# Kernel tuning notes

Hardware: AMD Instinct MI355X
Metric: run time of the kernel (lower is better)

Reference implementation:

```python
import jax, jax.numpy as jnp
import numpy as np
from jax import lax

NEG = -1e9
B, H, C, TX, TY = 4, 256, 80, 256, 1024  # batch, hidden, mel bins, text len, mel len


def setup_inputs() -> dict:
    key = jax.random.key(0)
    k = jax.random.split(key, 6)
    en = jax.random.normal(k[0], (B, H, TX), jnp.float32)
    mu = jax.random.normal(k[1], (B, C, TX), jnp.float32)
    log_sigma = 0.1 * jax.random.normal(k[2], (B, C, TX), jnp.float32)
    y = jax.random.normal(k[3], (B, C, TY), jnp.float32)
    x_lengths = jax.random.randint(k[4], (B,), TX // 2, TX + 1, jnp.int32)
    y_lengths = jax.random.randint(k[5], (B,), TY // 2, TY + 1, jnp.int32)
    return {"en": en, "mu": mu, "log_sigma": log_sigma, "y": y,
            "x_lengths": x_lengths, "y_lengths": y_lengths}


def sequence_mask(lengths, max_len):
    return jnp.arange(max_len)[None, :] < lengths[:, None]


def compute_log_probs(mu, log_sigma, y):
    # y: [B,C,Ty] -> [B,1,Ty,C]; mu/log_sigma: [B,C,Tx] -> [B,Tx,1,C]
    yb = jnp.transpose(y, (0, 2, 1))[:, None]
    mub = jnp.transpose(mu, (0, 2, 1))[:, :, None]
    lsb = jnp.transpose(log_sigma, (0, 2, 1))[:, :, None]
    # mse / sigma^2 = (y-mu)^2 * exp(-2*log_sigma); mean over channel dim
    expo = -0.5 * jnp.mean((yb - mub) ** 2 * jnp.exp(-2.0 * lsb), axis=-1)  # [B,Tx,Ty]
    return expo - 0.5 * jnp.mean(lsb, axis=-1)  # broadcast [B,Tx,1] -> [B,Tx,Ty]


def maximum_path(logp, mask, x_lengths, y_lengths):
    """Monotonic alignment search (Glow-TTS Viterbi DP), vectorized over batch."""
    b, tx, ty = logp.shape
    lp = jnp.where(mask > 0, logp, NEG)
    cols = jnp.moveaxis(lp, 2, 0)  # [Ty, B, Tx]
    v0 = jnp.broadcast_to(jnp.where(jnp.arange(tx) == 0, 0.0, NEG), (b, tx)).astype(logp.dtype)

    def fwd(v, col):
        v_shift = jnp.concatenate([jnp.full((b, 1), NEG, v.dtype), v[:, :-1]], axis=1)
        diag = v_shift > v  # come from (x-1, y-1) rather than (x, y-1)
        return col + jnp.maximum(v, v_shift), diag

    _, diags = lax.scan(fwd, v0, cols)  # diags: [Ty, B, Tx] bool

    xs_idx = jnp.arange(tx)

    def bwd(idx, inp):
        yv, dcol = inp
        active = yv < y_lengths  # [B]
        row = (xs_idx[None, :] == idx[:, None]) & active[:, None]
        d = jnp.take_along_axis(dcol, idx[:, None], axis=1)[:, 0]
        idx = jnp.where(active & (idx > 0) & d, idx - 1, idx)
        return idx, row

    _, rows = lax.scan(bwd, x_lengths - 1, (jnp.arange(ty), diags), reverse=True)
    return lax.stop_gradient(jnp.moveaxis(rows, 0, 2).astype(logp.dtype))  # [B,Tx,Ty]


def generate_path(dr, mask):
    # dr: [B,Tx] durations; mask: [B,Tx,Ty]
    ty = mask.shape[-1]
    cum = jnp.cumsum(dr, axis=1)
    pm = (jnp.arange(ty)[None, None, :] < cum[:, :, None]).astype(dr.dtype)
    path = pm - jnp.pad(pm, ((0, 0), (1, 0), (0, 0)))[:, :-1]
    return path * mask


def reference(en, mu, log_sigma, y, x_lengths, y_lengths):
    tx, ty = mu.shape[-1], y.shape[-1]
    x_mask = sequence_mask(x_lengths, tx).astype(jnp.float32)  # [B,Tx]
    y_mask = sequence_mask(y_lengths, ty).astype(jnp.float32)  # [B,Ty]
    attn_mask = x_mask[:, :, None] * y_mask[:, None, :]        # [B,Tx,Ty]
    logp = compute_log_probs(mu, log_sigma, y)
    attn = maximum_path(logp, attn_mask, x_lengths, y_lengths)
    dr_mas = jnp.sum(attn, axis=-1)                            # durations [B,Tx]
    path = generate_path(dr_mas, attn_mask)                    # convert_dr_to_align
    # expand_encoder_outputs: attn^T @ en^T -> [B,H,Ty]
    o_en_ex = jnp.einsum('bxy,bhx->bhy', path, en)
    return o_en_ex, logp, attn, dr_mas
```

## Files before the change

kernel.cpp:

```cpp
#include <hip/hip_runtime.h>
#include <cstdint>
#include <cmath>

#define B_ 4
#define H_ 256
#define C_ 80
#define TX_ 256
#define TY_ 1024
#define NC_ 64
#define NEGF (-1e9f)

#define OFF_LOGP (B_*H_*TY_)
#define OFF_ATTN (OFF_LOGP + B_*TX_*TY_)
#define OFF_DR   (OFF_ATTN + B_*TX_*TY_)

__device__ __forceinline__ float dpp_shr1_negfill_f32(float x) {
  union { float f; int i; } u, o, r;
  u.f = x; o.f = NEGF;
  r.i = __builtin_amdgcn_update_dpp(o.i, u.i, 0x138, 0xf, 0xf, false);
  return r.f;
}

__global__ __launch_bounds__(256) void k_logp(
    const float* __restrict__ mu, const float* __restrict__ ls,
    const float* __restrict__ y, const int* __restrict__ xlp,
    const int* __restrict__ ylp, float* __restrict__ logp_out,
    float* __restrict__ lpT)
{
  const int b  = blockIdx.y;
  const int x0 = blockIdx.x * 4;
  const int tid = threadIdx.x;
  __shared__ double s_w[4][C_];
  __shared__ double s_m1[4][C_];
  __shared__ double s_wm2[4][C_];
  __shared__ double s_lsv[4][C_];
  __shared__ double s_K[4];
  __shared__ double s_t0[4];
  __shared__ float tile[TY_][4];
  for (int i = tid; i < 4 * C_; i += 256) {
    int xi = i / C_, c = i - xi * C_;
    double m = (double)mu[(b * C_ + c) * TX_ + x0 + xi];
    double l = (double)ls[(b * C_ + c) * TX_ + x0 + xi];
    double w = exp(-2.0 * l);
    s_w[xi][c]   = w;
    s_m1[xi][c]  = -2.0 * w * m;
    s_wm2[xi][c] = w * m * m;
    s_lsv[xi][c] = l;
  }
  __syncthreads();
  {
    int xi = tid >> 6, cc = tid & 63;
    double kp = (cc < C_) ? s_wm2[xi][cc] : 0.0;
    double tp = (cc < C_) ? s_lsv[xi][cc] : 0.0;
    if (cc + 64 < C_) { kp += s_wm2[xi][cc + 64]; tp += s_lsv[xi][cc + 64]; }
#pragma unroll
    for (int off = 32; off; off >>= 1) {
      kp += __shfl_down(kp, off);
      tp += __shfl_down(tp, off);
    }
    if (cc == 0) { s_K[xi] = kp; s_t0[xi] = -0.5 * (tp * (1.0 / C_)); }
  }
  __syncthreads();

  const int t0 = tid * 4;
  double acc[4][4];
#pragma unroll
  for (int xi = 0; xi < 4; ++xi)
#pragma unroll
    for (int k = 0; k < 4; ++k) acc[xi][k] = 0.0;

  const float4* yp = (const float4*)(y + (size_t)b * C_ * TY_) + tid;
#pragma unroll 4
  for (int c = 0; c < C_; ++c) {
    float4 yv = yp[c * (TY_ / 4)];
    double y0 = yv.x, y1 = yv.y, y2 = yv.z, y3 = yv.w;
#pragma unroll
    for (int xi = 0; xi < 4; ++xi) {
      double w = s_w[xi][c], m1 = s_m1[xi][c];
      double u0 = fma(w, y0, m1), u1 = fma(w, y1, m1);
      double u2 = fma(w, y2, m1), u3 = fma(w, y3, m1);
      acc[xi][0] = fma(u0, y0, acc[xi][0]);
      acc[xi][1] = fma(u1, y1, acc[xi][1]);
      acc[xi][2] = fma(u2, y2, acc[xi][2]);
      acc[xi][3] = fma(u3, y3, acc[xi][3]);
    }
  }

  const int xlen = xlp[b], ylen = ylp[b];
#pragma unroll
  for (int xi = 0; xi < 4; ++xi) {
    int x = x0 + xi;
    double c0 = s_t0[xi], K = s_K[xi];
    float r[4];
#pragma unroll
    for (int k = 0; k < 4; ++k)
      r[k] = (float)((acc[xi][k] + K) * (-0.5 / C_) + c0);
    *(float4*)&logp_out[((size_t)(b * TX_ + x)) * TY_ + t0] =
        make_float4(r[0], r[1], r[2], r[3]);
    bool xm = x < xlen;
#pragma unroll
    for (int k = 0; k < 4; ++k)
      tile[t0 + k][xi] = (xm && (t0 + k) < ylen) ? r[k] : NEGF;
  }
  __syncthreads();

  float* dst = lpT + (size_t)b * TY_ * TX_ + x0;
  const float4* tp = (const float4*)tile;
#pragma unroll
  for (int k = 0; k < 4; ++k) {
    int t = tid + 256 * k;
    *(float4*)&dst[(size_t)t * TX_] = tp[t];
  }
}

__global__ __launch_bounds__(64, 1) void k_dp(
    const float* __restrict__ lpT, const int* __restrict__ xlp,
    const int* __restrict__ ylp, float* __restrict__ dr_out,
    int* __restrict__ cum_ws, int* __restrict__ xt_ws)
{
  const int b = blockIdx.x;
  const int lane = threadIdx.x;
  __shared__ uint32_t bits[8192];
  __shared__ uint32_t dur[TX_];

  const float4* src = (const float4*)(lpT + (size_t)b * TY_ * TX_) + lane;

  float v0 = (lane == 0) ? 0.0f : NEGF, v1 = NEGF, v2 = NEGF, v3 = NEGF;
  float sh = NEGF;
  uint32_t b0 = 0, b1 = 0, b2 = 0, b3 = 0;

  float4 BA[16], BB[16], BC[16];
#pragma unroll
  for (int i = 0; i < 16; ++i) BA[i] = src[i * 64];
#pragma unroll
  for (int i = 0; i < 16; ++i) BB[i] = src[(16 + i) * 64];

#define DP_BODY(CUR, LD, c)                                                  \
  {                                                                          \
    const int tl = ((c) + 2 < NC_ ? (c) + 2 : NC_ - 1) * 16;                 \
    _Pragma("unroll")                                                        \
    for (int i = 0; i < 16; ++i) LD[i] = src[(tl + i) * 64];                 \
    _Pragma("unroll")                                                        \
    for (int i = 0; i < 16; ++i) {                                           \
      const int t = (c) * 16 + i;                                            \
      const float vs0 = sh;                                                  \
      uint32_t bit = 1u << (t & 31);                                         \
      if (vs0 > v0) b0 |= bit;                                               \
      if (v0 > v1)  b1 |= bit;                                               \
      if (v1 > v2)  b2 |= bit;                                               \
      if (v2 > v3)  b3 |= bit;                                               \
      float nv3 = CUR[i].w + fmaxf(v3, v2);                                  \
      sh = dpp_shr1_negfill_f32(nv3);                                        \
      float nv2 = CUR[i].z + fmaxf(v2, v1);                                  \
      float nv1 = CUR[i].y + fmaxf(v1, v0);                                  \
      float nv0 = CUR[i].x + fmaxf(v0, vs0);                                 \
      v0 = nv0; v1 = nv1; v2 = nv2; v3 = nv3;                                \
      if ((t & 31) == 31) {                                                  \
        int w = t >> 5;                                                      \
        uint4 pk; pk.x = b0; pk.y = b1; pk.z = b2; pk.w = b3;                \
        *(uint4*)&bits[w * 256 + 4 * lane] = pk;                             \
        b0 = b1 = b2 = b3 = 0;                                               \
      }                                                                      \
    }                                                                        \
  }

  for (int c = 0; c < NC_; c += 3) {
    DP_BODY(BA, BC, c);
    if (c + 1 < NC_) DP_BODY(BB, BA, c + 1);
    if (c + 2 < NC_) DP_BODY(BC, BB, c + 2);
  }
#undef DP_BODY

#pragma unroll
  for (int j = 0; j < 4; ++j) dur[4 * lane + j] = 0;
  __syncthreads();

  const int xlen = xlp[b], ylen = ylp[b];
  if (lane == 0) {
    int idx = xlen - 1;
    int t = ylen - 1;
    while (t >= 0) {
      if (idx == 0) { dur[0] += (uint32_t)(t + 1); break; }
      int w = t >> 5, rr = t & 31;
      uint32_t word = bits[w * 256 + idx];
      word &= (rr == 31) ? 0xffffffffu : ((1u << (rr + 1)) - 1u);
      while (word == 0 && w > 0) { --w; word = bits[w * 256 + idx]; }
      if (word == 0) { dur[idx] += (uint32_t)(t + 1); break; }
      int bitpos = 31 - __builtin_clz(word);
      int tp = (w << 5) | bitpos;
      dur[idx] += (uint32_t)(t - tp + 1);
      --idx;
      t = tp - 1;
    }
  }
  __syncthreads();

  uint32_t d0 = dur[4 * lane], d1 = dur[4 * lane + 1];
  uint32_t d2 = dur[4 * lane + 2], d3 = dur[4 * lane + 3];
  uint32_t own = d0 + d1 + d2 + d3;
  uint32_t s = own;
#pragma unroll
  for (int off = 1; off < 64; off <<= 1) {
    uint32_t n = __shfl_up(s, off);
    if (lane >= off) s += n;
  }
  uint32_t base = s - own;
  uint32_t c0 = base + d0, c1 = c0 + d1, c2 = c1 + d2, c3 = c2 + d3;
  int x = 4 * lane;
  cum_ws[b * TX_ + x]     = (int)c0;
  cum_ws[b * TX_ + x + 1] = (int)c1;
  cum_ws[b * TX_ + x + 2] = (int)c2;
  cum_ws[b * TX_ + x + 3] = (int)c3;
  dr_out[b * TX_ + x]     = (float)d0;
  dr_out[b * TX_ + x + 1] = (float)d1;
  dr_out[b * TX_ + x + 2] = (float)d2;
  dr_out[b * TX_ + x + 3] = (float)d3;
  int* xt = xt_ws + b * TY_;
  for (uint32_t t = c0 - d0; t < c0; ++t) xt[t] = x;
  for (uint32_t t = c1 - d1; t < c1; ++t) xt[t] = x + 1;
  for (uint32_t t = c2 - d2; t < c2; ++t) xt[t] = x + 2;
  for (uint32_t t = c3 - d3; t < c3; ++t) xt[t] = x + 3;
}

__global__ __launch_bounds__(256) void k_epi(
    const int* __restrict__ cum_ws, const int* __restrict__ xt_ws,
    const float* __restrict__ en, const int* __restrict__ ylp,
    float* __restrict__ attn, float* __restrict__ oen)
{
  const int b = blockIdx.y, bx = blockIdx.x, tid = threadIdx.x;
  __shared__ float row[TX_];
  if (bx < TX_) {
    const int x = bx;
    int hi = cum_ws[b * TX_ + x];
    int lo = (x > 0) ? cum_ws[b * TX_ + x - 1] : 0;
    int t0 = tid * 4;
    float4 v;
    v.x = (t0     >= lo && t0     < hi) ? 1.f : 0.f;
    v.y = (t0 + 1 >= lo && t0 + 1 < hi) ? 1.f : 0.f;
    v.z = (t0 + 2 >= lo && t0 + 2 < hi) ? 1.f : 0.f;
    v.w = (t0 + 3 >= lo && t0 + 3 < hi) ? 1.f : 0.f;
    *(float4*)&attn[((size_t)(b * TX_ + x)) * TY_ + t0] = v;
  } else {
    const int h = bx - TX_;
    row[tid] = en[((size_t)(b * H_ + h)) * TX_ + tid];
    __syncthreads();
    const int ylen = ylp[b];
    int t0 = tid * 4;
    int4 xi = *(const int4*)&xt_ws[b * TY_ + t0];
    float4 v;
    v.x = (t0     < ylen) ? row[xi.x & (TX_ - 1)] : 0.f;
    v.y = (t0 + 1 < ylen) ? row[xi.y & (TX_ - 1)] : 0.f;
    v.z = (t0 + 2 < ylen) ? row[xi.z & (TX_ - 1)] : 0.f;
    v.w = (t0 + 3 < ylen) ? row[xi.w & (TX_ - 1)] : 0.f;
    *(float4*)&oen[((size_t)(b * H_ + h)) * TY_ + t0] = v;
  }
}

extern "C" void kernel_launch(void* const* d_in, const int* in_sizes, int n_in,
                              void* d_out, int out_size, void* d_ws, size_t ws_size,
                              hipStream_t stream)
{
  const float* en = (const float*)d_in[0];
  const float* mu = (const float*)d_in[1];
  const float* ls = (const float*)d_in[2];
  const float* y  = (const float*)d_in[3];
  const int*   xl = (const int*)d_in[4];
  const int*   yl = (const int*)d_in[5];

  float* out  = (float*)d_out;
  float* oen  = out;
  float* logp = out + OFF_LOGP;
  float* attn = out + OFF_ATTN;
  float* dr   = out + OFF_DR;

  int* cum = (int*)d_ws;
  int* xt  = cum + B_ * TX_;

  k_logp<<<dim3(TX_ / 4, B_),   256, 0, stream>>>(mu, ls, y, xl, yl, logp, attn);
  k_dp  <<<B_,                   64, 0, stream>>>(attn, xl, yl, dr, cum, xt);
  k_epi <<<dim3(TX_ + H_, B_),  256, 0, stream>>>(cum, xt, en, yl, attn, oen);
}
```

Before: 203.9 us.

## Hand-schedule DP prefetch with inline-asm loads into reserved VGPR banks

Replaces the compiler-scheduled triple-buffered float4 prefetch in the Viterbi DP kernel with inline-asm global_load_dwordx4 into two fixed banks of 64 VGPRs each (v128-v255), gated by explicit s_waitcnt vmcnt counts. Each 16-step chunk is copied out of its bank into a register array before the bank is refilled, so one chunk stays in flight while the current one is consumed. The goal is to keep memory latency off the serial DP recurrence without the compiler inserting conservative waits. In exchange it adds v_mov copy overhead, relies on hardcoded register clobbers and wait counts, and is fragile if the compiler's own loads change vmcnt accounting.

```diff
diff --git a/kernel.cpp b/kernel.cpp
--- a/kernel.cpp
+++ b/kernel.cpp
@@ -113,6 +113,98 @@
   }
 }
 
+#define ALLBANKS \
+  "v128","v129","v130","v131","v132","v133","v134","v135", \
+  "v136","v137","v138","v139","v140","v141","v142","v143", \
+  "v144","v145","v146","v147","v148","v149","v150","v151", \
+  "v152","v153","v154","v155","v156","v157","v158","v159", \
+  "v160","v161","v162","v163","v164","v165","v166","v167", \
+  "v168","v169","v170","v171","v172","v173","v174","v175", \
+  "v176","v177","v178","v179","v180","v181","v182","v183", \
+  "v184","v185","v186","v187","v188","v189","v190","v191", \
+  "v192","v193","v194","v195","v196","v197","v198","v199", \
+  "v200","v201","v202","v203","v204","v205","v206","v207", \
+  "v208","v209","v210","v211","v212","v213","v214","v215", \
+  "v216","v217","v218","v219","v220","v221","v222","v223", \
+  "v224","v225","v226","v227","v228","v229","v230","v231", \
+  "v232","v233","v234","v235","v236","v237","v238","v239", \
+  "v240","v241","v242","v243","v244","v245","v246","v247", \
+  "v248","v249","v250","v251","v252","v253","v254","v255"
+
+#define ISSUE_BANK(R0,R1,R2,R3)                                             \
+  asm volatile(                                                             \
+    "global_load_dwordx4 v[" #R0 ":" #R0 "+3], %0, off\n\t"                 \
+    "global_load_dwordx4 v[" #R0 "+4:" #R0 "+7], %0, off offset:1024\n\t"   \
+    "global_load_dwordx4 v[" #R0 "+8:" #R0 "+11], %0, off offset:2048\n\t"  \
+    "global_load_dwordx4 v[" #R0 "+12:" #R0 "+15], %0, off offset:3072\n\t" \
+    "global_load_dwordx4 v[" #R1 ":" #R1 "+3], %1, off\n\t"                 \
+    "global_load_dwordx4 v[" #R1 "+4:" #R1 "+7], %1, off offset:1024\n\t"   \
+    "global_load_dwordx4 v[" #R1 "+8:" #R1 "+11], %1, off offset:2048\n\t"  \
+    "global_load_dwordx4 v[" #R1 "+12:" #R1 "+15], %1, off offset:3072\n\t" \
+    "global_load_dwordx4 v[" #R2 ":" #R2 "+3], %2, off\n\t"                 \
+    "global_load_dwordx4 v[" #R2 "+4:" #R2 "+7], %2, off offset:1024\n\t"   \
+    "global_load_dwordx4 v[" #R2 "+8:" #R2 "+11], %2, off offset:2048\n\t"  \
+    "global_load_dwordx4 v[" #R2 "+12:" #R2 "+15], %2, off offset:3072\n\t" \
+    "global_load_dwordx4 v[" #R3 ":" #R3 "+3], %3, off\n\t"                 \
+    "global_load_dwordx4 v[" #R3 "+4:" #R3 "+7], %3, off offset:1024\n\t"   \
+    "global_load_dwordx4 v[" #R3 "+8:" #R3 "+11], %3, off offset:2048\n\t"  \
+    "global_load_dwordx4 v[" #R3 "+12:" #R3 "+15], %3, off offset:3072\n\t" \
+    :: "v"(q0), "v"(q1), "v"(q2), "v"(q3) : ALLBANKS)
+
+#define ISSUE_B0() ISSUE_BANK(128, 144, 160, 176)
+#define ISSUE_B1() ISSUE_BANK(192, 208, 224, 240)
+
+#define CP16(WAITSTR, R, c, o)                                              \
+  asm volatile(WAITSTR                                                      \
+    "v_mov_b32 %0, v[" #R "]\n\t"   "v_mov_b32 %1, v[" #R "+1]\n\t"         \
+    "v_mov_b32 %2, v[" #R "+2]\n\t" "v_mov_b32 %3, v[" #R "+3]\n\t"         \
+    "v_mov_b32 %4, v[" #R "+4]\n\t" "v_mov_b32 %5, v[" #R "+5]\n\t"         \
+    "v_mov_b32 %6, v[" #R "+6]\n\t" "v_mov_b32 %7, v[" #R "+7]\n\t"         \
+    "v_mov_b32 %8, v[" #R "+8]\n\t" "v_mov_b32 %9, v[" #R "+9]\n\t"         \
+    "v_mov_b32 %10, v[" #R "+10]\n\t" "v_mov_b32 %11, v[" #R "+11]\n\t"     \
+    "v_mov_b32 %12, v[" #R "+12]\n\t" "v_mov_b32 %13, v[" #R "+13]\n\t"     \
+    "v_mov_b32 %14, v[" #R "+14]\n\t" "v_mov_b32 %15, v[" #R "+15]"         \
+    : "=v"((c)[(o)+0]), "=v"((c)[(o)+1]), "=v"((c)[(o)+2]), "=v"((c)[(o)+3]),\
+      "=v"((c)[(o)+4]), "=v"((c)[(o)+5]), "=v"((c)[(o)+6]), "=v"((c)[(o)+7]),\
+      "=v"((c)[(o)+8]), "=v"((c)[(o)+9]), "=v"((c)[(o)+10]),"=v"((c)[(o)+11]),\
+      "=v"((c)[(o)+12]),"=v"((c)[(o)+13]),"=v"((c)[(o)+14]),"=v"((c)[(o)+15])\
+    :: ALLBANKS)
+
+#define COPYOUT_B0(WAITSTR, c)                                              \
+  CP16(WAITSTR, 128, c, 0);  CP16("", 144, c, 16);                          \
+  CP16("", 160, c, 32);      CP16("", 176, c, 48)
+#define COPYOUT_B1(WAITSTR, c)                                              \
+  CP16(WAITSTR, 192, c, 0);  CP16("", 208, c, 16);                          \
+  CP16("", 224, c, 32);      CP16("", 240, c, 48)
+
+#define ADV() { q0 += 4096; q1 += 4096; q2 += 4096; q3 += 4096; }
+
+#define CONSUME16C(c, k)                                                    \
+  {                                                                         \
+    const int sb = ((k) & 1) << 4;                                          \
+    _Pragma("unroll")                                                       \
+    for (int i = 0; i < 16; ++i) {                                          \
+      const float vs0 = sh;                                                 \
+      const uint32_t bit = 1u << (sb + i);                                  \
+      if (vs0 > v0) b0 |= bit;                                              \
+      if (v0 > v1)  b1 |= bit;                                              \
+      if (v1 > v2)  b2 |= bit;                                              \
+      if (v2 > v3)  b3 |= bit;                                              \
+      float nv3 = (c)[4*i+3] + fmaxf(v3, v2);                               \
+      sh = dpp_shr1_negfill_f32(nv3);                                       \
+      float nv2 = (c)[4*i+2] + fmaxf(v2, v1);                               \
+      float nv1 = (c)[4*i+1] + fmaxf(v1, v0);                               \
+      float nv0 = (c)[4*i+0] + fmaxf(v0, vs0);                              \
+      v0 = nv0; v1 = nv1; v2 = nv2; v3 = nv3;                               \
+    }                                                                       \
+    if ((k) & 1) {                                                          \
+      const int w = (k) >> 1;                                               \
+      uint4 pk; pk.x = b0; pk.y = b1; pk.z = b2; pk.w = b3;                 \
+      *(uint4*)&bits[w * 256 + 4 * lane] = pk;                              \
+      b0 = b1 = b2 = b3 = 0;                                                \
+    }                                                                       \
+  }
+
 __global__ __launch_bounds__(64, 1) void k_dp(
     const float* __restrict__ lpT, const int* __restrict__ xlp,
     const int* __restrict__ ylp, float* __restrict__ dr_out,
@@ -123,53 +215,32 @@
   __shared__ uint32_t bits[8192];
   __shared__ uint32_t dur[TX_];
 
-  const float4* src = (const float4*)(lpT + (size_t)b * TY_ * TX_) + lane;
+  const float* q0 = lpT + (size_t)b * TY_ * TX_ + 4 * lane;
+  const float* q1 = q0 + 1024;
+  const float* q2 = q0 + 2048;
+  const float* q3 = q0 + 3072;
 
   float v0 = (lane == 0) ? 0.0f : NEGF, v1 = NEGF, v2 = NEGF, v3 = NEGF;
   float sh = NEGF;
   uint32_t b0 = 0, b1 = 0, b2 = 0, b3 = 0;
-
-  float4 BA[16], BB[16], BC[16];
-#pragma unroll
-  for (int i = 0; i < 16; ++i) BA[i] = src[i * 64];
-#pragma unroll
-  for (int i = 0; i < 16; ++i) BB[i] = src[(16 + i) * 64];
-
-#define DP_BODY(CUR, LD, c)                                                  \
-  {                                                                          \
-    const int tl = ((c) + 2 < NC_ ? (c) + 2 : NC_ - 1) * 16;                 \
-    _Pragma("unroll")                                                        \
-    for (int i = 0; i < 16; ++i) LD[i] = src[(tl + i) * 64];                 \
-    _Pragma("unroll")                                                        \
-    for (int i = 0; i < 16; ++i) {                                           \
-      const int t = (c) * 16 + i;                                            \
-      const float vs0 = sh;                                                  \
-      uint32_t bit = 1u << (t & 31);                                         \
-      if (vs0 > v0) b0 |= bit;                                               \
-      if (v0 > v1)  b1 |= bit;                                               \
-      if (v1 > v2)  b2 |= bit;                                               \
-      if (v2 > v3)  b3 |= bit;                                               \
-      float nv3 = CUR[i].w + fmaxf(v3, v2);                                  \
-      sh = dpp_shr1_negfill_f32(nv3);                                        \
-      float nv2 = CUR[i].z + fmaxf(v2, v1);                                  \
-      float nv1 = CUR[i].y + fmaxf(v1, v0);                                  \
-      float nv0 = CUR[i].x + fmaxf(v0, vs0);                                 \
-      v0 = nv0; v1 = nv1; v2 = nv2; v3 = nv3;                                \
-      if ((t & 31) == 31) {                                                  \
-        int w = t >> 5;                                                      \
-        uint4 pk; pk.x = b0; pk.y = b1; pk.z = b2; pk.w = b3;                \
-        *(uint4*)&bits[w * 256 + 4 * lane] = pk;                             \
-        b0 = b1 = b2 = b3 = 0;                                               \
-      }                                                                      \
-    }                                                                        \
-  }
-
-  for (int c = 0; c < NC_; c += 3) {
-    DP_BODY(BA, BC, c);
-    if (c + 1 < NC_) DP_BODY(BB, BA, c + 1);
-    if (c + 2 < NC_) DP_BODY(BC, BB, c + 2);
-  }
-#undef DP_BODY
+  float c[64];
+
+  ISSUE_B0(); ADV();
+  ISSUE_B1(); ADV();
+
+  for (int p = 0; p < 62; p += 2) {
+    COPYOUT_B0("s_waitcnt vmcnt(16)\n\t", c);
+    ISSUE_B0(); ADV();
+    CONSUME16C(c, p);
+    COPYOUT_B1("s_waitcnt vmcnt(16)\n\t", c);
+    ISSUE_B1(); ADV();
+    CONSUME16C(c, p + 1);
+  }
+  COPYOUT_B0("s_waitcnt vmcnt(16)\n\t", c);
+  CONSUME16C(c, 62);
+  COPYOUT_B1("s_waitcnt vmcnt(0)\n\t", c);
+  CONSUME16C(c, 63);
+  asm volatile("s_waitcnt vmcnt(0)" ::: "memory");
 
 #pragma unroll
   for (int j = 0; j < 4; ++j) dur[4 * lane + j] = 0;
```

New measurement: 198.2 us. 2.8% less time.

## Wavefront-pipeline Viterbi DP across four waves with LDS boundary exchange

Applied to the files above, without the earlier changes.

The DP kernel goes from one 64-lane wave handling 4 text positions per lane to 256 threads with one text position each. The four waves work as a skewed pipeline over 16-step time chunks: each wave hands the values at its last lane to the next wave through a double-buffered LDS array and a barrier every phase. The aim is to shorten the serial per-step dependency chain and spread the global loads over more waves. In exchange it pays 69 workgroup barriers plus LDS traffic and a short pipeline fill and drain.

```diff
diff --git a/kernel.cpp b/kernel.cpp
--- a/kernel.cpp
+++ b/kernel.cpp
@@ -113,113 +113,121 @@
   }
 }
 
-__global__ __launch_bounds__(64, 1) void k_dp(
+#define PHASE_BAR() \
+  asm volatile("s_waitcnt lgkmcnt(0)\n\ts_barrier" ::: "memory")
+
+#define PHASEQ(FL, FC, q)                                                   \
+  {                                                                         \
+    const int cl = (q) - w;                                                 \
+    if (cl >= 0 && cl < NC_) {                                              \
+      const float* cb = gb + (size_t)cl * 16 * TX_ + tid;                   \
+      _Pragma("unroll")                                                     \
+      for (int i = 0; i < 16; ++i) FL[i] = cb[i * TX_];                     \
+    }                                                                       \
+    const int cc = (q) - 2 - w;                                             \
+    if (cc >= 0 && cc < NC_) {                                              \
+      if (cc == 0) { v = (tid == 0) ? 0.0f : NEGF; word = 0u; }             \
+      const uint32_t bitbase = 1u << ((cc & 1) << 4);                       \
+      float* wr = (lane == 63) ? &bdry[cc & 1][w + 1][0] : &dummy[lane];    \
+      const float* bp = &bdry[cc & 1][w][0];                                \
+      float bv[16];                                                         \
+      *(float4*)&bv[0]  = *(const float4*)(bp);                             \
+      *(float4*)&bv[4]  = *(const float4*)(bp + 4);                         \
+      *(float4*)&bv[8]  = *(const float4*)(bp + 8);                         \
+      *(float4*)&bv[12] = *(const float4*)(bp + 12);                        \
+      wr[0] = v;                                                            \
+      _Pragma("unroll")                                                     \
+      for (int i = 0; i < 16; ++i) {                                        \
+        float vl = dpp_shr1_negfill_f32(v);                                 \
+        if (amlane0) vl = bv[i];                                            \
+        if (vl > v) word |= (bitbase << i);                                 \
+        float nv = FC[i] + fmaxf(v, vl);                                    \
+        if (i < 15) wr[i + 1] = nv;                                         \
+        v = nv;                                                             \
+      }                                                                     \
+      if (cc & 1) { bits[(cc >> 1) * 256 + tid] = word; word = 0u; }        \
+    }                                                                       \
+    PHASE_BAR();                                                            \
+  }
+
+__global__ __launch_bounds__(256, 1) void k_dp(
     const float* __restrict__ lpT, const int* __restrict__ xlp,
     const int* __restrict__ ylp, float* __restrict__ dr_out,
     int* __restrict__ cum_ws, int* __restrict__ xt_ws)
 {
   const int b = blockIdx.x;
-  const int lane = threadIdx.x;
+  const int tid = threadIdx.x;
+  const int lane = tid & 63;
+  const int w = tid >> 6;
   __shared__ uint32_t bits[8192];
   __shared__ uint32_t dur[TX_];
-
-  const float4* src = (const float4*)(lpT + (size_t)b * TY_ * TX_) + lane;
-
-  float v0 = (lane == 0) ? 0.0f : NEGF, v1 = NEGF, v2 = NEGF, v3 = NEGF;
-  float sh = NEGF;
-  uint32_t b0 = 0, b1 = 0, b2 = 0, b3 = 0;
-
-  float4 BA[16], BB[16], BC[16];
-#pragma unroll
-  for (int i = 0; i < 16; ++i) BA[i] = src[i * 64];
-#pragma unroll
-  for (int i = 0; i < 16; ++i) BB[i] = src[(16 + i) * 64];
-
-#define DP_BODY(CUR, LD, c)                                                  \
-  {                                                                          \
-    const int tl = ((c) + 2 < NC_ ? (c) + 2 : NC_ - 1) * 16;                 \
-    _Pragma("unroll")                                                        \
-    for (int i = 0; i < 16; ++i) LD[i] = src[(tl + i) * 64];                 \
-    _Pragma("unroll")                                                        \
-    for (int i = 0; i < 16; ++i) {                                           \
-      const int t = (c) * 16 + i;                                            \
-      const float vs0 = sh;                                                  \
-      uint32_t bit = 1u << (t & 31);                                         \
-      if (vs0 > v0) b0 |= bit;                                               \
-      if (v0 > v1)  b1 |= bit;                                               \
-      if (v1 > v2)  b2 |= bit;                                               \
-      if (v2 > v3)  b3 |= bit;                                               \
-      float nv3 = CUR[i].w + fmaxf(v3, v2);                                  \
-      sh = dpp_shr1_negfill_f32(nv3);                                        \
-      float nv2 = CUR[i].z + fmaxf(v2, v1);                                  \
-      float nv1 = CUR[i].y + fmaxf(v1, v0);                                  \
-      float nv0 = CUR[i].x + fmaxf(v0, vs0);                                 \
-      v0 = nv0; v1 = nv1; v2 = nv2; v3 = nv3;                                \
-      if ((t & 31) == 31) {                                                  \
-        int w = t >> 5;                                                      \
-        uint4 pk; pk.x = b0; pk.y = b1; pk.z = b2; pk.w = b3;                \
-        *(uint4*)&bits[w * 256 + 4 * lane] = pk;                             \
-        b0 = b1 = b2 = b3 = 0;                                               \
-      }                                                                      \
-    }                                                                        \
-  }
-
-  for (int c = 0; c < NC_; c += 3) {
-    DP_BODY(BA, BC, c);
-    if (c + 1 < NC_) DP_BODY(BB, BA, c + 1);
-    if (c + 2 < NC_) DP_BODY(BC, BB, c + 2);
-  }
-#undef DP_BODY
-
-#pragma unroll
-  for (int j = 0; j < 4; ++j) dur[4 * lane + j] = 0;
+  __shared__ float bdry[2][5][16];
+  __shared__ float dummy[80];
+
+  const float* gb = lpT + (size_t)b * TY_ * TX_;
+  const bool amlane0 = (w > 0) && (lane == 0);
+
+  float v = NEGF;
+  uint32_t word = 0;
+  float f0[16], f1[16], f2[16];
+
+  for (int q = 0; q < 69; q += 3) {
+    PHASEQ(f0, f1, q);
+    PHASEQ(f1, f2, q + 1);
+    PHASEQ(f2, f0, q + 2);
+  }
+  __syncthreads();
+
+  dur[tid] = 0;
   __syncthreads();
 
   const int xlen = xlp[b], ylen = ylp[b];
-  if (lane == 0) {
+  if (tid == 0) {
     int idx = xlen - 1;
     int t = ylen - 1;
     while (t >= 0) {
-      if (idx == 0) { dur[0] += (uint32_t)(t + 1); break; }
-      int w = t >> 5, rr = t & 31;
-      uint32_t word = bits[w * 256 + idx];
-      word &= (rr == 31) ? 0xffffffffu : ((1u << (rr + 1)) - 1u);
-      while (word == 0 && w > 0) { --w; word = bits[w * 256 + idx]; }
-      if (word == 0) { dur[idx] += (uint32_t)(t + 1); break; }
-      int bitpos = 31 - __builtin_clz(word);
-      int tp = (w << 5) | bitpos;
-      dur[idx] += (uint32_t)(t - tp + 1);
+      if (idx == 0) { dur[0] = (uint32_t)(t + 1); break; }
+      int ww = t >> 5, rr = t & 31;
+      uint32_t wd = bits[ww * 256 + idx];
+      wd &= (rr == 31) ? 0xffffffffu : ((1u << (rr + 1)) - 1u);
+      while (wd == 0 && ww > 0) { --ww; wd = bits[ww * 256 + idx]; }
+      if (wd == 0) { dur[idx] = (uint32_t)(t + 1); break; }
+      int bitpos = 31 - __builtin_clz(wd);
+      int tp = (ww << 5) | bitpos;
+      dur[idx] = (uint32_t)(t - tp + 1);
       --idx;
       t = tp - 1;
     }
   }
   __syncthreads();
 
-  uint32_t d0 = dur[4 * lane], d1 = dur[4 * lane + 1];
-  uint32_t d2 = dur[4 * lane + 2], d3 = dur[4 * lane + 3];
-  uint32_t own = d0 + d1 + d2 + d3;
-  uint32_t s = own;
-#pragma unroll
-  for (int off = 1; off < 64; off <<= 1) {
-    uint32_t n = __shfl_up(s, off);
-    if (lane >= off) s += n;
-  }
-  uint32_t base = s - own;
-  uint32_t c0 = base + d0, c1 = c0 + d1, c2 = c1 + d2, c3 = c2 + d3;
-  int x = 4 * lane;
-  cum_ws[b * TX_ + x]     = (int)c0;
-  cum_ws[b * TX_ + x + 1] = (int)c1;
-  cum_ws[b * TX_ + x + 2] = (int)c2;
-  cum_ws[b * TX_ + x + 3] = (int)c3;
-  dr_out[b * TX_ + x]     = (float)d0;
-  dr_out[b * TX_ + x + 1] = (float)d1;
-  dr_out[b * TX_ + x + 2] = (float)d2;
-  dr_out[b * TX_ + x + 3] = (float)d3;
-  int* xt = xt_ws + b * TY_;
-  for (uint32_t t = c0 - d0; t < c0; ++t) xt[t] = x;
-  for (uint32_t t = c1 - d1; t < c1; ++t) xt[t] = x + 1;
-  for (uint32_t t = c2 - d2; t < c2; ++t) xt[t] = x + 2;
-  for (uint32_t t = c3 - d3; t < c3; ++t) xt[t] = x + 3;
+  if (w == 0) {
+    uint32_t d0 = dur[4 * lane], d1 = dur[4 * lane + 1];
+    uint32_t d2 = dur[4 * lane + 2], d3 = dur[4 * lane + 3];
+    uint32_t own = d0 + d1 + d2 + d3;
+    uint32_t s = own;
+#pragma unroll
+    for (int off = 1; off < 64; off <<= 1) {
+      uint32_t n = __shfl_up(s, off);
+      if (lane >= off) s += n;
+    }
+    uint32_t base = s - own;
+    uint32_t c0 = base + d0, c1 = c0 + d1, c2 = c1 + d2, c3 = c2 + d3;
+    int x = 4 * lane;
+    cum_ws[b * TX_ + x]     = (int)c0;
+    cum_ws[b * TX_ + x + 1] = (int)c1;
+    cum_ws[b * TX_ + x + 2] = (int)c2;
+    cum_ws[b * TX_ + x + 3] = (int)c3;
+    dr_out[b * TX_ + x]     = (float)d0;
+    dr_out[b * TX_ + x + 1] = (float)d1;
+    dr_out[b * TX_ + x + 2] = (float)d2;
+    dr_out[b * TX_ + x + 3] = (float)d3;
+    int* xt = xt_ws + b * TY_;
+    for (uint32_t t = c0 - d0; t < c0; ++t) xt[t] = x;
+    for (uint32_t t = c1 - d1; t < c1; ++t) xt[t] = x + 1;
+    for (uint32_t t = c2 - d2; t < c2; ++t) xt[t] = x + 2;
+    for (uint32_t t = c3 - d3; t < c3; ++t) xt[t] = x + 3;
+  }
 }
 
 __global__ __launch_bounds__(256) void k_epi(
@@ -277,6 +285,6 @@
   int* xt  = cum + B_ * TX_;
 
   k_logp<<<dim3(TX_ / 4, B_),   256, 0, stream>>>(mu, ls, y, xl, yl, logp, attn);
-  k_dp  <<<B_,                   64, 0, stream>>>(attn, xl, yl, dr, cum, xt);
+  k_dp  <<<B_,                  256, 0, stream>>>(attn, xl, yl, dr, cum, xt);
   k_epi <<<dim3(TX_ + H_, B_),  256, 0, stream>>>(cum, xt, en, yl, attn, oen);
 }
```

Result: faster. 188.1 us (-7.7%).
